# Kernel optimization log

Measured on AMD Instinct MI355X. Metric: run time of the kernel, lower is better.

Reference implementation:

```python
import jax, jax.numpy as jnp
import numpy as np

NUM_CODES = 4096
CODE_DIM = 256
COMMITMENT_COST = 0.25
DIVERSITY_WEIGHT = 0.1
B = 65536


def setup_inputs() -> dict:
    key = jax.random.key(0)
    kz, ke = jax.random.split(key)
    z = jax.random.normal(kz, (B, CODE_DIM), dtype=jnp.float32)
    embedding = jax.random.normal(ke, (NUM_CODES, CODE_DIM), dtype=jnp.float32)
    return {"z": z, "embedding": embedding}


def reference(z, embedding):
    # distances [B, K] = ||z||^2 + ||e||^2 - 2 z e^T
    distances = (
        jnp.sum(z * z, axis=1, keepdims=True)
        + jnp.sum(embedding * embedding, axis=1)
        - 2.0 * z @ embedding.T
    )
    indices = jnp.argmin(distances, axis=1)  # [B] int
    z_q = embedding[indices]                  # [B, D]

    sg = jax.lax.stop_gradient
    commitment_loss = jnp.mean((z - sg(z_q)) ** 2)
    embedding_loss = jnp.mean((sg(z) - z_q) ** 2)

    # diversity regularizer over soft assignments
    soft = jax.nn.softmax(-distances, axis=1)        # [B, K]
    avg_soft = jnp.mean(soft, axis=0)                # [K]
    entropy = -jnp.sum(avg_soft * jnp.log(avg_soft + 1e-10))
    max_entropy = jnp.log(jnp.float32(NUM_CODES))
    diversity_loss = max_entropy - entropy

    vq_loss = (
        commitment_loss * COMMITMENT_COST
        + embedding_loss
        + DIVERSITY_WEIGHT * diversity_loss
    )

    # straight-through estimator
    z_q_st = z + sg(z_q - z)

    # perplexity from hard assignments (bincount == one-hot mean)
    avg_probs = jnp.bincount(indices, length=NUM_CODES).astype(jnp.float32) / B
    perplexity = jnp.exp(-jnp.sum(avg_probs * jnp.log(avg_probs + 1e-10)))

    return (z_q_st, vq_loss, perplexity, indices, diversity_loss)
```

## Files before the change

### kernel.cpp

```cpp
#include <hip/hip_runtime.h>
#include <cstdint>
#include <cstddef>


#define NROWS     65536
#define NCODES    4096
#define DDIM      256
#define CAND_CAP  24
#define MARGIN    2.0f
#define SKIP_THR  17.0f

typedef _Float16 half8 __attribute__((ext_vector_type(8)));
typedef _Float16 half4 __attribute__((ext_vector_type(4)));
typedef float    f32x4 __attribute__((ext_vector_type(4)));

#define WS_BINCNT   0u
#define WS_ZERO_END 16384u
#define WS_CANDCNT  16384u
#define WS_SPART    278528u
#define WS_EF16     8667136u
#define WS_EE       10764288u
#define WS_ROWD     10780672u
#define WS_CANDIDX  11042816u
#define WS_TE       17334272u
#define WS_TP       17367040u
#define WS_END      17399808u

__device__ __forceinline__ void gload_lds16(const void* g, void* lds) {
    __builtin_amdgcn_global_load_lds(
        (const __attribute__((address_space(1))) unsigned int*)g,
        (__attribute__((address_space(3))) unsigned int*)lds, 16, 0, 0);
}

__global__ __launch_bounds__(256)
void prep_kernel(const float* __restrict__ src, _Float16* __restrict__ dst,
                 float* __restrict__ norms)
{
    const int tid = threadIdx.x;
    const int w = tid >> 6, l = tid & 63;
    const int row = blockIdx.x * 4 + w;
    const float4 v = *(const float4*)(src + (size_t)row * DDIM + l * 4);
    half4 h;
    h[0] = (_Float16)v.x; h[1] = (_Float16)v.y;
    h[2] = (_Float16)v.z; h[3] = (_Float16)v.w;
    *(half4*)(dst + (size_t)row * DDIM + l * 4) = h;
    double s = (double)v.x * v.x + (double)v.y * v.y
             + (double)v.z * v.z + (double)v.w * v.w;
#pragma unroll
    for (int off = 1; off < 64; off <<= 1) s += __shfl_xor(s, off, 64);
    if (l == 0) norms[row] = (float)s;
}

__global__ __launch_bounds__(256, 2)
void sweep_fused_kernel(const float* __restrict__ z, const _Float16* __restrict__ ef,
                        const float* __restrict__ ee, float* __restrict__ Spart,
                        int* __restrict__ cand_cnt, int* __restrict__ cand_idx)
{
    __shared__ _Float16 Bl[2][64 * 256];
    __shared__ float Sl[NCODES];

    const int tid = threadIdx.x;
    const int w = tid >> 6, l = tid & 63;
    const int lg = l >> 4, lc = l & 15;
    const int row0 = blockIdx.x * 128;

    half8 af[2][8];
#pragma unroll
    for (int fr = 0; fr < 2; ++fr)
#pragma unroll
    for (int ksl = 0; ksl < 8; ++ksl) {
        const float* zp = z + (size_t)(row0 + w * 32 + fr * 16 + lc) * DDIM + ksl * 32 + lg * 8;
        const float4 v0 = *(const float4*)zp;
        const float4 v1 = *(const float4*)(zp + 4);
        half8 h;
        h[0] = (_Float16)v0.x; h[1] = (_Float16)v0.y; h[2] = (_Float16)v0.z; h[3] = (_Float16)v0.w;
        h[4] = (_Float16)v1.x; h[5] = (_Float16)v1.y; h[6] = (_Float16)v1.z; h[7] = (_Float16)v1.w;
        af[fr][ksl] = h;
    }

    for (int i = tid; i < NCODES; i += 256) Sl[i] = 0.0f;

    int soff[8];
#pragma unroll
    for (int it = 0; it < 8; ++it) {
        const int it_g = w * 8 + it;
        const int ksl = it_g >> 2, cf = it_g & 3;
        soff[it] = (cf * 16 + lc) * 512 + ksl * 64 + lg * 16;
    }
    const char* efb = (const char*)ef;
    char* blb = (char*)&Bl[0][0];

    float pm[8], pZ[8];
#pragma unroll
    for (int i = 0; i < 8; ++i) { pm[i] = 1e30f; pZ[i] = 0.0f; }
    int bcnt[8];
#pragma unroll
    for (int i = 0; i < 8; ++i) bcnt[i] = 0;

#pragma unroll
    for (int it = 0; it < 8; ++it)
        gload_lds16(efb + soff[it], blb + (w * 8 + it) * 1024);
    __syncthreads();

    for (int s = 0; s < 128; ++s) {
        const int cur = s & 1;
        const int nt = s & 63;

        float eevc[4];
#pragma unroll
        for (int cf = 0; cf < 4; ++cf) eevc[cf] = ee[nt * 64 + cf * 16 + lc];

        if (s < 127) {
            const int nnt = (s + 1) & 63;
            const char* src = efb + ((size_t)nnt << 15);
            char* dst = blb + (cur ^ 1) * 32768;
#pragma unroll
            for (int it = 0; it < 8; ++it)
                gload_lds16(src + soff[it], dst + (w * 8 + it) * 1024);
        }

        f32x4 acc[2][4];
#pragma unroll
        for (int fr = 0; fr < 2; ++fr)
#pragma unroll
            for (int cf = 0; cf < 4; ++cf) acc[fr][cf] = (f32x4){0.f, 0.f, 0.f, 0.f};

        const char* bb = blb + cur * 32768 + (l << 4);
#pragma unroll
        for (int ksl = 0; ksl < 8; ++ksl) {
#pragma unroll
            for (int cf = 0; cf < 4; ++cf) {
                const half8 b = *(const half8*)(bb + (ksl * 4 + cf) * 1024);
                acc[0][cf] = __builtin_amdgcn_mfma_f32_16x16x32_f16(af[0][ksl], b, acc[0][cf], 0, 0, 0);
                acc[1][cf] = __builtin_amdgcn_mfma_f32_16x16x32_f16(af[1][ksl], b, acc[1][cf], 0, 0, 0);
            }
        }

        if (s < 64) {
#pragma unroll
            for (int fr = 0; fr < 2; ++fr)
#pragma unroll
            for (int reg = 0; reg < 4; ++reg) {
                const int ri = fr * 4 + reg;
                const float d0 = fmaf(-2.0f, acc[fr][0][reg], eevc[0]);
                const float d1 = fmaf(-2.0f, acc[fr][1][reg], eevc[1]);
                const float d2 = fmaf(-2.0f, acc[fr][2][reg], eevc[2]);
                const float d3 = fmaf(-2.0f, acc[fr][3][reg], eevc[3]);
                const float mloc = fminf(fminf(d0, d1), fminf(d2, d3));
                float m = pm[ri];
                if (mloc < m + SKIP_THR) {
                    if (mloc < m) { pZ[ri] *= __expf(mloc - m); m = mloc; pm[ri] = m; }
                    pZ[ri] += __expf(m - d0) + __expf(m - d1) + __expf(m - d2) + __expf(m - d3);
                }
            }
        } else {
            float sp[4] = {0.f, 0.f, 0.f, 0.f};
#pragma unroll
            for (int fr = 0; fr < 2; ++fr)
#pragma unroll
            for (int reg = 0; reg < 4; ++reg) {
                const int ri = fr * 4 + reg;
                const float m = pm[ri], iz = pZ[ri];
#pragma unroll
                for (int cf = 0; cf < 4; ++cf) {
                    const float d = fmaf(-2.0f, acc[fr][cf][reg], eevc[cf]);
                    const bool hit = (d <= m + MARGIN);
                    const unsigned long long mk = __ballot(hit);
                    if (mk) {
                        const unsigned grp = (unsigned)((mk >> (lg * 16)) & 0xFFFFull);
                        const int slot = bcnt[ri] + __popc(grp & ((1u << lc) - 1u));
                        if (hit && slot < CAND_CAP) {
                            const int rg_ = row0 + w * 32 + fr * 16 + lg * 4 + reg;
                            cand_idx[(size_t)rg_ * CAND_CAP + slot] = nt * 64 + cf * 16 + lc;
                        }
                        bcnt[ri] += __popc(grp);
                    }
                    if (d <= m + SKIP_THR) sp[cf] += __expf(m - d) * iz;
                }
            }
#pragma unroll
            for (int cf = 0; cf < 4; ++cf) {
                float v = sp[cf];
                v += __shfl_xor(v, 16, 64);
                v += __shfl_xor(v, 32, 64);
                if (l < 16) atomicAdd(&Sl[nt * 64 + cf * 16 + l], v);
            }
        }

        if (s == 63) {
#pragma unroll
            for (int ri = 0; ri < 8; ++ri) {
                float m = pm[ri], Zv = pZ[ri];
#pragma unroll
                for (int off = 1; off < 16; off <<= 1) {
                    const float mo = __shfl_xor(m, off, 64);
                    const float Zo = __shfl_xor(Zv, off, 64);
                    const float mn = fminf(m, mo);
                    Zv = Zv * __expf(mn - m) + Zo * __expf(mn - mo);
                    m = mn;
                }
                pm[ri] = m;
                pZ[ri] = 1.0f / Zv;
            }
        }

        __syncthreads();
    }

    if (lc == 0) {
#pragma unroll
        for (int fr = 0; fr < 2; ++fr)
#pragma unroll
        for (int reg = 0; reg < 4; ++reg)
            cand_cnt[row0 + w * 32 + fr * 16 + lg * 4 + reg] = bcnt[fr * 4 + reg];
    }

    for (int i = tid; i < NCODES; i += 256)
        Spart[(size_t)blockIdx.x * NCODES + i] = Sl[i];
}

__global__ __launch_bounds__(256)
void refine_kernel(const float* __restrict__ z, const float* __restrict__ emb,
                   const int* __restrict__ cand_cnt, const int* __restrict__ cand_idx,
                   float* __restrict__ out_zq, float* __restrict__ out_idx,
                   unsigned int* __restrict__ bincnt, float* __restrict__ rowD)
{
    const int tid = threadIdx.x;
    const int w = tid >> 6, l = tid & 63;
    const int row = blockIdx.x * 4 + w;
    const float4 zv = *(const float4*)(z + (size_t)row * DDIM + l * 4);
    const double z0 = zv.x, z1 = zv.y, z2 = zv.z, z3 = zv.w;
    const int craw = cand_cnt[row];
    const int cnt = craw < 1 ? 1 : (craw > CAND_CAP ? CAND_CAP : craw);
    double dmin = 1e300; int kmin = 0;
    for (int c = 0; c < cnt; ++c) {
        int k = (craw < 1) ? 0 : cand_idx[(size_t)row * CAND_CAP + c];
        k &= (NCODES - 1);
        const float4 ev = *(const float4*)(emb + (size_t)k * DDIM + l * 4);
        const double t0 = z0 - ev.x, t1 = z1 - ev.y, t2 = z2 - ev.z, t3 = z3 - ev.w;
        double s = t0 * t0 + t1 * t1 + t2 * t2 + t3 * t3;
#pragma unroll
        for (int off = 1; off < 64; off <<= 1) s += __shfl_xor(s, off, 64);
        if (s < dmin || (s == dmin && k < kmin)) { dmin = s; kmin = k; }
    }
    const float4 bv = *(const float4*)(emb + (size_t)kmin * DDIM + l * 4);
    *(float4*)(out_zq + (size_t)row * DDIM + l * 4) = bv;
    if (l == 0) {
        out_idx[row] = (float)kmin;
        atomicAdd(&bincnt[kmin], 1u);
        rowD[row] = (float)dmin;
    }
}

__global__ __launch_bounds__(256)
void reduce1_kernel(const float* __restrict__ Spart, const unsigned int* __restrict__ bincnt,
                    const float* __restrict__ rowD,
                    double* __restrict__ te, double* __restrict__ tp, double* __restrict__ tm)
{
    const int k = blockIdx.x * 256 + threadIdx.x;
    double s = 0.0;
#pragma unroll 8
    for (int wg = 0; wg < 512; ++wg) s += (double)Spart[(size_t)wg * NCODES + k];
    const double avg = s * (1.0 / 65536.0);
    te[k] = avg * log(avg + 1e-10);
    const double ap = (double)bincnt[k] * (1.0 / 65536.0);
    tp[k] = ap * log(ap + 1e-10);
    double dm = 0.0;
#pragma unroll
    for (int j = 0; j < 16; ++j) dm += (double)rowD[k * 16 + j];
    tm[k] = dm;
}

__global__ __launch_bounds__(256)
void reduce2_kernel(const double* __restrict__ te, const double* __restrict__ tp,
                    const double* __restrict__ tm, float* __restrict__ out)
{
    __shared__ double sa[256], sb[256], sc[256];
    const int tid = threadIdx.x;
    double a = 0.0, b = 0.0, c = 0.0;
    for (int i = tid; i < NCODES; i += 256) { a += te[i]; b += tp[i]; c += tm[i]; }
    sa[tid] = a; sb[tid] = b; sc[tid] = c;
    __syncthreads();
    for (int s = 128; s > 0; s >>= 1) {
        if (tid < s) { sa[tid] += sa[tid + s]; sb[tid] += sb[tid + s]; sc[tid] += sc[tid + s]; }
        __syncthreads();
    }
    if (tid == 0) {
        const double entropy    = -sa[0];
        const double diversity  = log(4096.0) - entropy;
        const double perplexity = exp(-sb[0]);
        const double mse        = sc[0] * (1.0 / 16777216.0);
        const double vq         = 1.25 * mse + 0.1 * diversity;
        out[16777216] = (float)vq;
        out[16777217] = (float)perplexity;
        out[16842754] = (float)diversity;
    }
}

extern "C" void kernel_launch(void* const* d_in, const int* in_sizes, int n_in,
                              void* d_out, int out_size, void* d_ws, size_t ws_size,
                              hipStream_t stream)
{
    const float* z   = (const float*)d_in[0];
    const float* emb = (const float*)d_in[1];
    float* out = (float*)d_out;
    char* ws = (char*)d_ws;
    if (ws_size < (size_t)WS_END) return;

    unsigned int* bincnt   = (unsigned int*)(ws + WS_BINCNT);
    int*          cand_cnt = (int*)(ws + WS_CANDCNT);
    float*        Spart    = (float*)(ws + WS_SPART);
    _Float16*     ef16     = (_Float16*)(ws + WS_EF16);
    float*        ee       = (float*)(ws + WS_EE);
    float*        rowD     = (float*)(ws + WS_ROWD);
    int*          cand_idx = (int*)(ws + WS_CANDIDX);
    double*       te       = (double*)(ws + WS_TE);
    double*       tp       = (double*)(ws + WS_TP);
    double*       tm       = (double*)(ws + WS_CANDIDX);

    hipMemsetAsync(d_ws, 0, WS_ZERO_END, stream);
    hipLaunchKernelGGL(prep_kernel, dim3(NCODES / 4), dim3(256), 0, stream, emb, ef16, ee);
    hipLaunchKernelGGL(sweep_fused_kernel, dim3(NROWS / 128), dim3(256), 0, stream,
                       z, ef16, ee, Spart, cand_cnt, cand_idx);
    hipLaunchKernelGGL(refine_kernel, dim3(NROWS / 4), dim3(256), 0, stream,
                       z, emb, cand_cnt, cand_idx, out, out + 16777218, bincnt, rowD);
    hipLaunchKernelGGL(reduce1_kernel, dim3(16), dim3(256), 0, stream, Spart, bincnt, rowD, te, tp, tm);
    hipLaunchKernelGGL(reduce2_kernel, dim3(1), dim3(256), 0, stream, te, tp, tm, out);
}
```

Baseline: 421.3 us.

## Halve codebook tile width, raise occupancy, fold norm bias into MFMA accumulator

The sweep kernel now streams 32-code tiles instead of 64, which halves LDS per block and the accumulator count, and asks for 3 blocks per CU instead of 2. The -0.5*||e||^2 term is preloaded into the MFMA accumulators and the softmax and candidate logic works on u = z·e - ||e||²/2, using max and exp(2·Δ), so the per-element fma is gone. The ee values for the next tile are prefetched one iteration ahead, and s_setprio is raised around the MFMA block. The cost is twice as many loop iterations and barriers for the same work.

Result: slower. 481.6 us (+14.3%).

```diff
diff --git a/kernel.cpp b/kernel.cpp
--- a/kernel.cpp
+++ b/kernel.cpp
@@ -7,8 +7,8 @@
 #define NCODES    4096
 #define DDIM      256
 #define CAND_CAP  24
-#define MARGIN    2.0f
-#define SKIP_THR  17.0f
+#define UMARGIN   1.0f
+#define USKIP     8.5f
 
 typedef _Float16 half8 __attribute__((ext_vector_type(8)));
 typedef _Float16 half4 __attribute__((ext_vector_type(4)));
@@ -51,12 +51,12 @@
     if (l == 0) norms[row] = (float)s;
 }
 
-__global__ __launch_bounds__(256, 2)
+__global__ __launch_bounds__(256, 3)
 void sweep_fused_kernel(const float* __restrict__ z, const _Float16* __restrict__ ef,
                         const float* __restrict__ ee, float* __restrict__ Spart,
                         int* __restrict__ cand_cnt, int* __restrict__ cand_idx)
 {
-    __shared__ _Float16 Bl[2][64 * 256];
+    __shared__ _Float16 Bl[2][32 * 256];
     __shared__ float Sl[NCODES];
 
     const int tid = threadIdx.x;
@@ -80,131 +80,138 @@
 
     for (int i = tid; i < NCODES; i += 256) Sl[i] = 0.0f;
 
-    int soff[8];
-#pragma unroll
-    for (int it = 0; it < 8; ++it) {
-        const int it_g = w * 8 + it;
-        const int ksl = it_g >> 2, cf = it_g & 3;
+    int soff[4];
+#pragma unroll
+    for (int it = 0; it < 4; ++it) {
+        const int it_g = w * 4 + it;
+        const int ksl = it_g >> 1, cf = it_g & 1;
         soff[it] = (cf * 16 + lc) * 512 + ksl * 64 + lg * 16;
     }
     const char* efb = (const char*)ef;
     char* blb = (char*)&Bl[0][0];
 
-    float pm[8], pZ[8];
-#pragma unroll
-    for (int i = 0; i < 8; ++i) { pm[i] = 1e30f; pZ[i] = 0.0f; }
+    float pmx[8], pZ[8];
+#pragma unroll
+    for (int i = 0; i < 8; ++i) { pmx[i] = -1e30f; pZ[i] = 0.0f; }
     int bcnt[8];
 #pragma unroll
     for (int i = 0; i < 8; ++i) bcnt[i] = 0;
 
-#pragma unroll
-    for (int it = 0; it < 8; ++it)
-        gload_lds16(efb + soff[it], blb + (w * 8 + it) * 1024);
+    float eevc[2];
+#pragma unroll
+    for (int cf = 0; cf < 2; ++cf) eevc[cf] = ee[cf * 16 + lc];
+#pragma unroll
+    for (int it = 0; it < 4; ++it)
+        gload_lds16(efb + soff[it], blb + (w * 4 + it) * 1024);
     __syncthreads();
 
-    for (int s = 0; s < 128; ++s) {
+    for (int s = 0; s < 256; ++s) {
         const int cur = s & 1;
-        const int nt = s & 63;
-
-        float eevc[4];
-#pragma unroll
-        for (int cf = 0; cf < 4; ++cf) eevc[cf] = ee[nt * 64 + cf * 16 + lc];
-
-        if (s < 127) {
-            const int nnt = (s + 1) & 63;
-            const char* src = efb + ((size_t)nnt << 15);
-            char* dst = blb + (cur ^ 1) * 32768;
-#pragma unroll
-            for (int it = 0; it < 8; ++it)
-                gload_lds16(src + soff[it], dst + (w * 8 + it) * 1024);
-        }
-
-        f32x4 acc[2][4];
-#pragma unroll
-        for (int fr = 0; fr < 2; ++fr)
-#pragma unroll
-            for (int cf = 0; cf < 4; ++cf) acc[fr][cf] = (f32x4){0.f, 0.f, 0.f, 0.f};
-
-        const char* bb = blb + cur * 32768 + (l << 4);
+        const int nt = s & 127;
+        const int nnt = (s + 1) & 127;
+
+        float eevn[2];
+#pragma unroll
+        for (int cf = 0; cf < 2; ++cf) eevn[cf] = ee[nnt * 32 + cf * 16 + lc];
+
+        if (s < 255) {
+            const char* src = efb + ((size_t)nnt << 14);
+            char* dst = blb + (cur ^ 1) * 16384;
+#pragma unroll
+            for (int it = 0; it < 4; ++it)
+                gload_lds16(src + soff[it], dst + (w * 4 + it) * 1024);
+        }
+
+        const float eh0 = -0.5f * eevc[0], eh1 = -0.5f * eevc[1];
+        f32x4 acc[2][2];
+#pragma unroll
+        for (int fr = 0; fr < 2; ++fr) {
+            acc[fr][0] = (f32x4){eh0, eh0, eh0, eh0};
+            acc[fr][1] = (f32x4){eh1, eh1, eh1, eh1};
+        }
+
+        const char* bb = blb + cur * 16384 + (l << 4);
+        __builtin_amdgcn_s_setprio(1);
 #pragma unroll
         for (int ksl = 0; ksl < 8; ++ksl) {
-#pragma unroll
-            for (int cf = 0; cf < 4; ++cf) {
-                const half8 b = *(const half8*)(bb + (ksl * 4 + cf) * 1024);
-                acc[0][cf] = __builtin_amdgcn_mfma_f32_16x16x32_f16(af[0][ksl], b, acc[0][cf], 0, 0, 0);
-                acc[1][cf] = __builtin_amdgcn_mfma_f32_16x16x32_f16(af[1][ksl], b, acc[1][cf], 0, 0, 0);
-            }
-        }
-
-        if (s < 64) {
+            const half8 b0 = *(const half8*)(bb + (ksl * 2 + 0) * 1024);
+            const half8 b1 = *(const half8*)(bb + (ksl * 2 + 1) * 1024);
+#pragma unroll
+            for (int fr = 0; fr < 2; ++fr) {
+                acc[fr][0] = __builtin_amdgcn_mfma_f32_16x16x32_f16(af[fr][ksl], b0, acc[fr][0], 0, 0, 0);
+                acc[fr][1] = __builtin_amdgcn_mfma_f32_16x16x32_f16(af[fr][ksl], b1, acc[fr][1], 0, 0, 0);
+            }
+        }
+        __builtin_amdgcn_s_setprio(0);
+
+        if (s < 128) {
 #pragma unroll
             for (int fr = 0; fr < 2; ++fr)
 #pragma unroll
             for (int reg = 0; reg < 4; ++reg) {
                 const int ri = fr * 4 + reg;
-                const float d0 = fmaf(-2.0f, acc[fr][0][reg], eevc[0]);
-                const float d1 = fmaf(-2.0f, acc[fr][1][reg], eevc[1]);
-                const float d2 = fmaf(-2.0f, acc[fr][2][reg], eevc[2]);
-                const float d3 = fmaf(-2.0f, acc[fr][3][reg], eevc[3]);
-                const float mloc = fminf(fminf(d0, d1), fminf(d2, d3));
-                float m = pm[ri];
-                if (mloc < m + SKIP_THR) {
-                    if (mloc < m) { pZ[ri] *= __expf(mloc - m); m = mloc; pm[ri] = m; }
-                    pZ[ri] += __expf(m - d0) + __expf(m - d1) + __expf(m - d2) + __expf(m - d3);
+                const float u0 = acc[fr][0][reg];
+                const float u1 = acc[fr][1][reg];
+                const float mloc = fmaxf(u0, u1);
+                float m = pmx[ri];
+                if (mloc > m - USKIP) {
+                    if (mloc > m) { pZ[ri] *= __expf(2.0f * (m - mloc)); m = mloc; pmx[ri] = m; }
+                    pZ[ri] += __expf(2.0f * (u0 - m)) + __expf(2.0f * (u1 - m));
                 }
             }
         } else {
-            float sp[4] = {0.f, 0.f, 0.f, 0.f};
+            float sp[2] = {0.f, 0.f};
 #pragma unroll
             for (int fr = 0; fr < 2; ++fr)
 #pragma unroll
             for (int reg = 0; reg < 4; ++reg) {
                 const int ri = fr * 4 + reg;
-                const float m = pm[ri], iz = pZ[ri];
-#pragma unroll
-                for (int cf = 0; cf < 4; ++cf) {
-                    const float d = fmaf(-2.0f, acc[fr][cf][reg], eevc[cf]);
-                    const bool hit = (d <= m + MARGIN);
+                const float m = pmx[ri], iz = pZ[ri];
+#pragma unroll
+                for (int cf = 0; cf < 2; ++cf) {
+                    const float u = acc[fr][cf][reg];
+                    const bool hit = (u >= m - UMARGIN);
                     const unsigned long long mk = __ballot(hit);
                     if (mk) {
                         const unsigned grp = (unsigned)((mk >> (lg * 16)) & 0xFFFFull);
                         const int slot = bcnt[ri] + __popc(grp & ((1u << lc) - 1u));
                         if (hit && slot < CAND_CAP) {
                             const int rg_ = row0 + w * 32 + fr * 16 + lg * 4 + reg;
-                            cand_idx[(size_t)rg_ * CAND_CAP + slot] = nt * 64 + cf * 16 + lc;
+                            cand_idx[(size_t)rg_ * CAND_CAP + slot] = nt * 32 + cf * 16 + lc;
                         }
                         bcnt[ri] += __popc(grp);
                     }
-                    if (d <= m + SKIP_THR) sp[cf] += __expf(m - d) * iz;
+                    if (u >= m - USKIP) sp[cf] += __expf(2.0f * (u - m)) * iz;
                 }
             }
 #pragma unroll
-            for (int cf = 0; cf < 4; ++cf) {
+            for (int cf = 0; cf < 2; ++cf) {
                 float v = sp[cf];
                 v += __shfl_xor(v, 16, 64);
                 v += __shfl_xor(v, 32, 64);
-                if (l < 16) atomicAdd(&Sl[nt * 64 + cf * 16 + l], v);
-            }
-        }
-
-        if (s == 63) {
+                if (l < 16) atomicAdd(&Sl[nt * 32 + cf * 16 + l], v);
+            }
+        }
+
+        if (s == 127) {
 #pragma unroll
             for (int ri = 0; ri < 8; ++ri) {
-                float m = pm[ri], Zv = pZ[ri];
+                float m = pmx[ri], Zv = pZ[ri];
 #pragma unroll
                 for (int off = 1; off < 16; off <<= 1) {
                     const float mo = __shfl_xor(m, off, 64);
                     const float Zo = __shfl_xor(Zv, off, 64);
-                    const float mn = fminf(m, mo);
-                    Zv = Zv * __expf(mn - m) + Zo * __expf(mn - mo);
+                    const float mn = fmaxf(m, mo);
+                    Zv = Zv * __expf(2.0f * (m - mn)) + Zo * __expf(2.0f * (mo - mn));
                     m = mn;
                 }
-                pm[ri] = m;
+                pmx[ri] = m;
                 pZ[ri] = 1.0f / Zv;
             }
         }
 
         __syncthreads();
+        eevc[0] = eevn[0]; eevc[1] = eevn[1];
     }
 
     if (lc == 0) {
```

## Switch sweep to 32x32x16 MFMA with log2-domain scores and bias-initialized accumulators

Applied to the files above, without the earlier changes.

The fused sweep kernel now uses 32x32x16 f16 MFMA tiles instead of 16x16x32, so each wave holds one 32-row fragment against two 32-code column blocks. z is pre-scaled by 2/ln2, and the accumulator starts at -ee/ln2, so the MFMA output is already the negated distance in log2 units and the online softmax can use exp2f without a separate fma. Code-norm loads are prefetched one step ahead. The cost is a different lane-to-row mapping for the ballot-based candidate collection, and an extra rounding of z*scale to fp16 that slightly changes precision.

Result: slower. 487.3 us (+15.7%).

```diff
diff --git a/kernel.cpp b/kernel.cpp
--- a/kernel.cpp
+++ b/kernel.cpp
@@ -7,12 +7,14 @@
 #define NCODES    4096
 #define DDIM      256
 #define CAND_CAP  24
-#define MARGIN    2.0f
-#define SKIP_THR  17.0f
+#define ZSCALE    2.8853900817779268f
+#define EECOEF    1.4426950408889634f
+#define VMARGIN   2.8853900817779268f
+#define VSKIP     24.525815695112378f
 
 typedef _Float16 half8 __attribute__((ext_vector_type(8)));
 typedef _Float16 half4 __attribute__((ext_vector_type(4)));
-typedef float    f32x4 __attribute__((ext_vector_type(4)));
+typedef float    f32x16 __attribute__((ext_vector_type(16)));
 
 #define WS_BINCNT   0u
 #define WS_ZERO_END 16384u
@@ -61,21 +63,22 @@
 
     const int tid = threadIdx.x;
     const int w = tid >> 6, l = tid & 63;
-    const int lg = l >> 4, lc = l & 15;
+    const int c31 = l & 31, lh = l >> 5;
     const int row0 = blockIdx.x * 128;
-
-    half8 af[2][8];
-#pragma unroll
-    for (int fr = 0; fr < 2; ++fr)
-#pragma unroll
-    for (int ksl = 0; ksl < 8; ++ksl) {
-        const float* zp = z + (size_t)(row0 + w * 32 + fr * 16 + lc) * DDIM + ksl * 32 + lg * 8;
+    const int rowb = row0 + w * 32;
+
+    half8 af[16];
+#pragma unroll
+    for (int q = 0; q < 16; ++q) {
+        const float* zp = z + (size_t)(rowb + c31) * DDIM + q * 16 + lh * 8;
         const float4 v0 = *(const float4*)zp;
         const float4 v1 = *(const float4*)(zp + 4);
         half8 h;
-        h[0] = (_Float16)v0.x; h[1] = (_Float16)v0.y; h[2] = (_Float16)v0.z; h[3] = (_Float16)v0.w;
-        h[4] = (_Float16)v1.x; h[5] = (_Float16)v1.y; h[6] = (_Float16)v1.z; h[7] = (_Float16)v1.w;
-        af[fr][ksl] = h;
+        h[0] = (_Float16)(v0.x * ZSCALE); h[1] = (_Float16)(v0.y * ZSCALE);
+        h[2] = (_Float16)(v0.z * ZSCALE); h[3] = (_Float16)(v0.w * ZSCALE);
+        h[4] = (_Float16)(v1.x * ZSCALE); h[5] = (_Float16)(v1.y * ZSCALE);
+        h[6] = (_Float16)(v1.z * ZSCALE); h[7] = (_Float16)(v1.w * ZSCALE);
+        af[q] = h;
     }
 
     for (int i = tid; i < NCODES; i += 256) Sl[i] = 0.0f;
@@ -83,20 +86,23 @@
     int soff[8];
 #pragma unroll
     for (int it = 0; it < 8; ++it) {
-        const int it_g = w * 8 + it;
-        const int ksl = it_g >> 2, cf = it_g & 3;
-        soff[it] = (cf * 16 + lc) * 512 + ksl * 64 + lg * 16;
+        const int fid = w * 8 + it;
+        const int q = fid >> 1, c = fid & 1;
+        soff[it] = (c * 32 + c31) * 512 + q * 32 + lh * 16;
     }
     const char* efb = (const char*)ef;
     char* blb = (char*)&Bl[0][0];
 
-    float pm[8], pZ[8];
-#pragma unroll
-    for (int i = 0; i < 8; ++i) { pm[i] = 1e30f; pZ[i] = 0.0f; }
-    int bcnt[8];
-#pragma unroll
-    for (int i = 0; i < 8; ++i) bcnt[i] = 0;
-
+    float pmx[16], pZ[16];
+#pragma unroll
+    for (int i = 0; i < 16; ++i) { pmx[i] = -1e30f; pZ[i] = 0.0f; }
+    int bcnt[16];
+#pragma unroll
+    for (int i = 0; i < 16; ++i) bcnt[i] = 0;
+
+    float eevc[2], eevn[2];
+#pragma unroll
+    for (int c = 0; c < 2; ++c) eevc[c] = ee[c * 32 + c31];
 #pragma unroll
     for (int it = 0; it < 8; ++it)
         gload_lds16(efb + soff[it], blb + (w * 8 + it) * 1024);
@@ -105,13 +111,12 @@
     for (int s = 0; s < 128; ++s) {
         const int cur = s & 1;
         const int nt = s & 63;
-
-        float eevc[4];
-#pragma unroll
-        for (int cf = 0; cf < 4; ++cf) eevc[cf] = ee[nt * 64 + cf * 16 + lc];
+        const int nnt = (s + 1) & 63;
+
+#pragma unroll
+        for (int c = 0; c < 2; ++c) eevn[c] = ee[nnt * 64 + c * 32 + c31];
 
         if (s < 127) {
-            const int nnt = (s + 1) & 63;
             const char* src = efb + ((size_t)nnt << 15);
             char* dst = blb + (cur ^ 1) * 32768;
 #pragma unroll
@@ -119,100 +124,92 @@
                 gload_lds16(src + soff[it], dst + (w * 8 + it) * 1024);
         }
 
-        f32x4 acc[2][4];
-#pragma unroll
-        for (int fr = 0; fr < 2; ++fr)
-#pragma unroll
-            for (int cf = 0; cf < 4; ++cf) acc[fr][cf] = (f32x4){0.f, 0.f, 0.f, 0.f};
+        const float ehA = -EECOEF * eevc[0], ehB = -EECOEF * eevc[1];
+        f32x16 accA, accB;
+#pragma unroll
+        for (int j = 0; j < 16; ++j) { accA[j] = ehA; accB[j] = ehB; }
 
         const char* bb = blb + cur * 32768 + (l << 4);
 #pragma unroll
-        for (int ksl = 0; ksl < 8; ++ksl) {
-#pragma unroll
-            for (int cf = 0; cf < 4; ++cf) {
-                const half8 b = *(const half8*)(bb + (ksl * 4 + cf) * 1024);
-                acc[0][cf] = __builtin_amdgcn_mfma_f32_16x16x32_f16(af[0][ksl], b, acc[0][cf], 0, 0, 0);
-                acc[1][cf] = __builtin_amdgcn_mfma_f32_16x16x32_f16(af[1][ksl], b, acc[1][cf], 0, 0, 0);
-            }
+        for (int q = 0; q < 16; ++q) {
+            const half8 b0 = *(const half8*)(bb + (q * 2 + 0) * 1024);
+            const half8 b1 = *(const half8*)(bb + (q * 2 + 1) * 1024);
+            accA = __builtin_amdgcn_mfma_f32_32x32x16_f16(af[q], b0, accA, 0, 0, 0);
+            accB = __builtin_amdgcn_mfma_f32_32x32x16_f16(af[q], b1, accB, 0, 0, 0);
         }
 
         if (s < 64) {
 #pragma unroll
-            for (int fr = 0; fr < 2; ++fr)
-#pragma unroll
-            for (int reg = 0; reg < 4; ++reg) {
-                const int ri = fr * 4 + reg;
-                const float d0 = fmaf(-2.0f, acc[fr][0][reg], eevc[0]);
-                const float d1 = fmaf(-2.0f, acc[fr][1][reg], eevc[1]);
-                const float d2 = fmaf(-2.0f, acc[fr][2][reg], eevc[2]);
-                const float d3 = fmaf(-2.0f, acc[fr][3][reg], eevc[3]);
-                const float mloc = fminf(fminf(d0, d1), fminf(d2, d3));
-                float m = pm[ri];
-                if (mloc < m + SKIP_THR) {
-                    if (mloc < m) { pZ[ri] *= __expf(mloc - m); m = mloc; pm[ri] = m; }
-                    pZ[ri] += __expf(m - d0) + __expf(m - d1) + __expf(m - d2) + __expf(m - d3);
+            for (int r = 0; r < 16; ++r) {
+                const float u0 = accA[r];
+                const float u1 = accB[r];
+                const float mloc = fmaxf(u0, u1);
+                float m = pmx[r];
+                if (mloc > m - VSKIP) {
+                    if (mloc > m) { pZ[r] *= exp2f(m - mloc); m = mloc; pmx[r] = m; }
+                    pZ[r] += exp2f(u0 - m) + exp2f(u1 - m);
                 }
             }
         } else {
-            float sp[4] = {0.f, 0.f, 0.f, 0.f};
-#pragma unroll
-            for (int fr = 0; fr < 2; ++fr)
-#pragma unroll
-            for (int reg = 0; reg < 4; ++reg) {
-                const int ri = fr * 4 + reg;
-                const float m = pm[ri], iz = pZ[ri];
-#pragma unroll
-                for (int cf = 0; cf < 4; ++cf) {
-                    const float d = fmaf(-2.0f, acc[fr][cf][reg], eevc[cf]);
-                    const bool hit = (d <= m + MARGIN);
+            float sp[2] = {0.f, 0.f};
+#pragma unroll
+            for (int r = 0; r < 16; ++r) {
+                const float m = pmx[r], iz = pZ[r];
+                const float u0 = accA[r];
+                const float u1 = accB[r];
+#pragma unroll
+                for (int c = 0; c < 2; ++c) {
+                    const float u = (c == 0) ? u0 : u1;
+                    const bool hit = (u >= m - VMARGIN);
                     const unsigned long long mk = __ballot(hit);
                     if (mk) {
-                        const unsigned grp = (unsigned)((mk >> (lg * 16)) & 0xFFFFull);
-                        const int slot = bcnt[ri] + __popc(grp & ((1u << lc) - 1u));
+                        const unsigned grp = (unsigned)(mk >> (lh * 32));
+                        const int slot = bcnt[r] + __popc(grp & ((1u << c31) - 1u));
                         if (hit && slot < CAND_CAP) {
-                            const int rg_ = row0 + w * 32 + fr * 16 + lg * 4 + reg;
-                            cand_idx[(size_t)rg_ * CAND_CAP + slot] = nt * 64 + cf * 16 + lc;
+                            const int rg_ = rowb + (r & 3) + 8 * (r >> 2) + 4 * lh;
+                            cand_idx[(size_t)rg_ * CAND_CAP + slot] = nt * 64 + c * 32 + c31;
                         }
-                        bcnt[ri] += __popc(grp);
+                        bcnt[r] += __popc(grp);
                     }
-                    if (d <= m + SKIP_THR) sp[cf] += __expf(m - d) * iz;
+                }
+                if (fmaxf(u0, u1) >= m - VSKIP) {
+                    sp[0] += exp2f(u0 - m) * iz;
+                    sp[1] += exp2f(u1 - m) * iz;
                 }
             }
 #pragma unroll
-            for (int cf = 0; cf < 4; ++cf) {
-                float v = sp[cf];
-                v += __shfl_xor(v, 16, 64);
+            for (int c = 0; c < 2; ++c) {
+                float v = sp[c];
                 v += __shfl_xor(v, 32, 64);
-                if (l < 16) atomicAdd(&Sl[nt * 64 + cf * 16 + l], v);
+                if (lh == 0) atomicAdd(&Sl[nt * 64 + c * 32 + c31], v);
             }
         }
 
         if (s == 63) {
 #pragma unroll
-            for (int ri = 0; ri < 8; ++ri) {
-                float m = pm[ri], Zv = pZ[ri];
-#pragma unroll
-                for (int off = 1; off < 16; off <<= 1) {
+            for (int r = 0; r < 16; ++r) {
+                float m = pmx[r], Zv = pZ[r];
+#pragma unroll
+                for (int off = 1; off < 32; off <<= 1) {
                     const float mo = __shfl_xor(m, off, 64);
                     const float Zo = __shfl_xor(Zv, off, 64);
-                    const float mn = fminf(m, mo);
-                    Zv = Zv * __expf(mn - m) + Zo * __expf(mn - mo);
+                    const float mn = fmaxf(m, mo);
+                    Zv = Zv * exp2f(m - mn) + Zo * exp2f(mo - mn);
                     m = mn;
                 }
-                pm[ri] = m;
-                pZ[ri] = 1.0f / Zv;
+                pmx[r] = m;
+                pZ[r] = 1.0f / Zv;
             }
         }
 
         __syncthreads();
-    }
-
-    if (lc == 0) {
-#pragma unroll
-        for (int fr = 0; fr < 2; ++fr)
-#pragma unroll
-        for (int reg = 0; reg < 4; ++reg)
-            cand_cnt[row0 + w * 32 + fr * 16 + lg * 4 + reg] = bcnt[fr * 4 + reg];
+        eevc[0] = eevn[0]; eevc[1] = eevn[1];
+    }
+
+    if (c31 == 0) {
+#pragma unroll
+        for (int r = 0; r < 16; ++r)
+            cand_cnt[rowb + (r & 3) + 8 * (r >> 2) + 4 * lh] = bcnt[r];
     }
 
     for (int i = tid; i < NCODES; i += 256)
```
